# Performance work log

Measured on AMD Instinct MI355X. Metric: run time of the kernel, lower is better.

Reference implementation:

```python
import jax, jax.numpy as jnp
import numpy as np

B, N, C, H, T = 64, 4096, 768, 12, 10


def setup_inputs() -> dict:
    key = jax.random.key(0)
    kx, kq, kk, kv, kp = jax.random.split(key, 5)
    std = 0.02  # trunc_normal std from _init_weights
    return {
        "x": jax.random.normal(kx, (B, N, C), jnp.float32),
        "Wq": std * jax.random.normal(kq, (C, C), jnp.float32),
        "Wk": std * jax.random.normal(kk, (C, C), jnp.float32),
        "Wv": std * jax.random.normal(kv, (C, C), jnp.float32),
        "Wp": std * jax.random.normal(kp, (C, C), jnp.float32),
        "bp": jnp.zeros((C,), jnp.float32),
        "nb_task_tokens": T,
    }


def reference(x, Wq, Wk, Wv, Wp, bp, nb_task_tokens):
    Bq, Nq, Cq = x.shape
    d = Cq // H
    scale = d ** -0.5
    Tt = nb_task_tokens
    # q only from the first T (task) tokens; k, v from all N tokens
    q = (x[:, :Tt] @ Wq).reshape(Bq, Tt, H, d).transpose(0, 2, 1, 3) * scale  # [B,H,T,d]
    k = (x @ Wk).reshape(Bq, Nq, H, d).transpose(0, 2, 1, 3)                  # [B,H,N,d]
    v = (x @ Wv).reshape(Bq, Nq, H, d).transpose(0, 2, 1, 3)                  # [B,H,N,d]
    attn = jnp.einsum("bhtd,bhnd->bhtn", q, k)                                # [B,H,T,N]
    # mask: task token i may attend to itself and to all patch tokens (cols >= T),
    # but not to other task tokens
    rows = jnp.arange(Tt)[:, None]
    cols = jnp.arange(Nq)[None, :]
    allowed = (cols >= Tt) | (cols == rows)                                   # [T,N]
    attn = jnp.where(allowed, attn, -jnp.inf)
    attn = jax.nn.softmax(attn, axis=-1)
    x_cls = jnp.einsum("bhtn,bhnd->bhtd", attn, v)                            # [B,H,T,d]
    x_cls = x_cls.transpose(0, 2, 1, 3).reshape(Bq, Tt, Cq)
    x_cls = x_cls @ Wp + bp
    return (x_cls, attn, v)
```

## Files before the change

### kernel.cpp

```cpp
#include <hip/hip_runtime.h>

typedef __attribute__((ext_vector_type(8))) short short8;
typedef __attribute__((ext_vector_type(4))) short short4v;
typedef __attribute__((ext_vector_type(4))) float f32x4;

__device__ __forceinline__ unsigned short f2bf(float f) {
  union { float f; unsigned u; } v; v.f = f;
  unsigned r = v.u + 0x7FFFu + ((v.u >> 16) & 1u);
  return (unsigned short)(r >> 16);
}

__device__ __forceinline__ void gload16(const void* g, void* l) {
  __builtin_amdgcn_global_load_lds(
      (const __attribute__((address_space(1))) void*)g,
      (__attribute__((address_space(3))) void*)l, 16, 0, 0);
}

__global__ __launch_bounds__(256) void conv_x(const float* __restrict__ x,
                                              unsigned short* __restrict__ xb) {
  const long total = 25165824;
  long stride = (long)gridDim.x * 256;
  for (long u = blockIdx.x * 256 + threadIdx.x; u < total; u += stride) {
    const float* p = x + u * 8;
    float4 a = *(const float4*)p;
    float4 b = *(const float4*)(p + 4);
    short8 h;
    h[0] = (short)f2bf(a.x); h[1] = (short)f2bf(a.y);
    h[2] = (short)f2bf(a.z); h[3] = (short)f2bf(a.w);
    h[4] = (short)f2bf(b.x); h[5] = (short)f2bf(b.y);
    h[6] = (short)f2bf(b.z); h[7] = (short)f2bf(b.w);
    *(short8*)(xb + u * 8) = h;
  }
}

__global__ __launch_bounds__(256) void prep_w(const float* __restrict__ Wk,
                                              const float* __restrict__ Wv,
                                              unsigned short* __restrict__ Wt) {
  int idx = blockIdx.x * 256 + threadIdx.x;
  int n = idx / 768, k = idx - n * 768;
  float w = (n < 768) ? Wk[k * 768 + n] : Wv[k * 768 + (n - 768)];
  Wt[idx] = f2bf(w);
}

__global__ __launch_bounds__(256) void q_proj(const float* __restrict__ x,
                                              const float* __restrict__ Wq,
                                              unsigned short* __restrict__ q_ws) {
  int b = blockIdx.x, tid = threadIdx.x;
  __shared__ float xr[7680];
  const float* xp = x + (long)b * 4096 * 768;
  for (int i = tid; i < 7680; i += 256) xr[i] = xp[i];
  for (int i = tid; i < 12 * 6 * 64; i += 256) {
    int h = i / 384, rem = i - h * 384;
    int t = 10 + rem / 64, d = rem & 63;
    q_ws[(((long)(b * 12 + h) * 16 + t) << 6) + d] = 0;
  }
  __syncthreads();
  float acc[10][3];
#pragma unroll
  for (int t = 0; t < 10; ++t) { acc[t][0] = 0.f; acc[t][1] = 0.f; acc[t][2] = 0.f; }
  for (int k = 0; k < 768; ++k) {
    const float* wr = Wq + (long)k * 768;
    float w0 = wr[tid], w1 = wr[tid + 256], w2 = wr[tid + 512];
#pragma unroll
    for (int t = 0; t < 10; ++t) {
      float xv = xr[t * 768 + k];
      acc[t][0] += xv * w0; acc[t][1] += xv * w1; acc[t][2] += xv * w2;
    }
  }
#pragma unroll
  for (int t = 0; t < 10; ++t) {
#pragma unroll
    for (int j = 0; j < 3; ++j) {
      int c = tid + j * 256;
      int h = c >> 6, d = c & 63;
      q_ws[(((long)(b * 12 + h) * 16 + t) << 6) + d] = f2bf(acc[t][j] * 0.125f);
    }
  }
}

__global__ __launch_bounds__(512, 2) void gemm_kv7(const unsigned short* __restrict__ xb,
                                                   const unsigned short* __restrict__ Wt,
                                                   unsigned short* __restrict__ k_ws,
                                                   float* __restrict__ v_out) {
  __shared__ char smem[98304];
#define AB(i) ((unsigned short*)(smem + (i) * 16384))

  int bid = blockIdx.x;
  int lb = (bid & 7) * 768 + (bid >> 3);
  int mt = lb / 6, nt = lb - mt * 6;
  long m0 = (long)mt * 256; int n0 = nt * 256;
  int tid = threadIdx.x, lane = tid & 63;
  int uw = __builtin_amdgcn_readfirstlane(tid >> 6);
  int wm = uw >> 2, wn = uw & 3;
  int r16 = lane & 15, gk = lane >> 4;

  const unsigned short* xs = xb + m0 * 768;
  const unsigned short* wp = Wt + (long)n0 * 768;

  int srow = lane >> 2;
  int schunk = ((lane & 3) ^ ((srow >> 1) & 3)) << 3;
  const unsigned short* pA = xs + (long)(uw * 16 + srow) * 768 + schunk;
  const unsigned short* pB = wp + (long)(uw * 16 + srow) * 768 + schunk;
  const long JROW = 128 * 768;

  int rc = (gk ^ ((r16 >> 1) & 3)) << 3;

  f32x4 acc[8][4];
#pragma unroll
  for (int i = 0; i < 8; ++i)
#pragma unroll
    for (int j = 0; j < 4; ++j) acc[i][j] = (f32x4){0.f, 0.f, 0.f, 0.f};

#define STAGE(BUF, OFF)                                                         \
  {                                                                             \
    gload16(pA + (OFF), AB(2 * (BUF)) + uw * 512);                              \
    gload16(pA + (OFF) + JROW, AB(2 * (BUF)) + uw * 512 + 4096);                \
    gload16(pB + (OFF), AB(2 * (BUF) + 1) + uw * 512);                          \
    gload16(pB + (OFF) + JROW, AB(2 * (BUF) + 1) + uw * 512 + 4096);            \
  }
#define COMPUTE(BUF)                                                            \
  {                                                                             \
    const unsigned short* Ab = AB(2 * (BUF));                                   \
    const unsigned short* Bb = AB(2 * (BUF) + 1);                               \
    short8 af[8], bfr[4];                                                       \
    _Pragma("unroll")                                                           \
    for (int mi = 0; mi < 8; ++mi)                                              \
      af[mi] = *(const short8*)&Ab[(wm * 128 + mi * 16 + r16) * 32 + rc];       \
    _Pragma("unroll")                                                           \
    for (int ni = 0; ni < 4; ++ni)                                              \
      bfr[ni] = *(const short8*)&Bb[(wn * 64 + ni * 16 + r16) * 32 + rc];       \
    _Pragma("unroll")                                                           \
    for (int mi = 0; mi < 8; ++mi)                                              \
      _Pragma("unroll")                                                         \
      for (int ni = 0; ni < 4; ++ni)                                            \
        acc[mi][ni] = __builtin_amdgcn_mfma_f32_16x16x32_bf16(af[mi], bfr[ni],  \
                                                              acc[mi][ni], 0, 0, 0); \
  }
#define WB4 asm volatile("s_waitcnt vmcnt(4) lgkmcnt(0)\n\ts_barrier" ::: "memory")
#define WB0 asm volatile("s_waitcnt vmcnt(0) lgkmcnt(0)\n\ts_barrier" ::: "memory")

  STAGE(0, 0);
  STAGE(1, 32);
  WB4;

#pragma unroll 1
  for (int g = 0; g < 7; ++g) {
    STAGE(2, 64);  COMPUTE(0); WB4;
    STAGE(0, 96);  COMPUTE(1); WB4;
    STAGE(1, 128); COMPUTE(2); WB4;
    pA += 96; pB += 96;
  }
  STAGE(2, 64); COMPUTE(0); WB4;
  COMPUTE(1); WB0;
  COMPUTE(2);

#undef STAGE
#undef COMPUTE
#undef WB4
#undef WB0

  float* scr = (float*)smem + uw * 1088;
  bool is_k = (n0 < 768);
  int h = (is_k ? (n0 >> 6) : ((n0 - 768) >> 6)) + wn;
  int bq = (int)(m0 >> 12);
  int nb = (int)(m0 & 4095) + wm * 128;

#pragma unroll
  for (int mi = 0; mi < 8; ++mi) {
#pragma unroll
    for (int ni = 0; ni < 4; ++ni)
#pragma unroll
      for (int r = 0; r < 4; ++r)
        scr[(gk * 4 + r) * 68 + ni * 16 + r16] = acc[mi][ni][r];
    int nbase = nb + mi * 16;
    if (is_k) {
#pragma unroll
      for (int p = 0; p < 2; ++p) {
        int row = p * 8 + (lane >> 3), d0 = (lane & 7) << 3;
        float4 aa = *(const float4*)&scr[row * 68 + d0];
        float4 bb = *(const float4*)&scr[row * 68 + d0 + 4];
        short8 hh;
        hh[0] = (short)f2bf(aa.x); hh[1] = (short)f2bf(aa.y);
        hh[2] = (short)f2bf(aa.z); hh[3] = (short)f2bf(aa.w);
        hh[4] = (short)f2bf(bb.x); hh[5] = (short)f2bf(bb.y);
        hh[6] = (short)f2bf(bb.z); hh[7] = (short)f2bf(bb.w);
        *(short8*)&k_ws[((long)(bq * 12 + h) * 4096 + nbase + row) * 64 + d0] = hh;
      }
    } else {
#pragma unroll
      for (int p = 0; p < 4; ++p) {
        int row = p * 4 + (lane >> 4), d0 = (lane & 15) << 2;
        float4 aa = *(const float4*)&scr[row * 68 + d0];
        *(float4*)&v_out[((long)(bq * 12 + h) * 4096 + nbase + row) * 64 + d0] = aa;
      }
    }
  }
#undef AB
}

__global__ __launch_bounds__(256) void gemm_kv(const float* __restrict__ x,
                                               const unsigned short* __restrict__ Wt,
                                               unsigned short* __restrict__ k_ws,
                                               float* __restrict__ v_out) {
  __shared__ char lds[32768];
  int bid = blockIdx.x;
  int lb = (bid & 7) * 3072 + (bid >> 3);
  int mt = lb / 12, nt = lb - mt * 12;
  long m0 = (long)mt * 128; int n0 = nt * 128;
  int tid = threadIdx.x, lane = tid & 63;
  int wid = tid >> 6, wm = wid >> 1, wn = wid & 1;
  int rlo = lane & 15, gk = lane >> 4;

  const float* xs = x + m0 * 768;
  const unsigned short* wp = Wt + (long)n0 * 768;

  int arow0 = tid >> 3, ak4 = (tid & 7) << 2;
  int bn = tid >> 1, bg = (tid & 1) << 1;

  f32x4 acc[4][4];
#pragma unroll
  for (int i = 0; i < 4; ++i)
#pragma unroll
    for (int j = 0; j < 4; ++j) acc[i][j] = (f32x4){0.f, 0.f, 0.f, 0.f};

  float4 fA[4]; short8 wB[2];
#pragma unroll
  for (int it = 0; it < 4; ++it) {
    int row = it * 32 + arow0;
    fA[it] = *(const float4*)(xs + (long)row * 768 + ak4);
  }
#pragma unroll
  for (int i = 0; i < 2; ++i)
    wB[i] = *(const short8*)(wp + (long)bn * 768 + (bg + i) * 8);
#pragma unroll
  for (int it = 0; it < 4; ++it) {
    int row = it * 32 + arow0;
    short4v h;
    h[0] = (short)f2bf(fA[it].x); h[1] = (short)f2bf(fA[it].y);
    h[2] = (short)f2bf(fA[it].z); h[3] = (short)f2bf(fA[it].w);
    *(short4v*)(lds + row * 64 + ((ak4 * 2) ^ (((row >> 1) & 3) << 4))) = h;
  }
#pragma unroll
  for (int i = 0; i < 2; ++i)
    *(short8*)(lds + 16384 + bn * 64 + (((bg + i) * 16) ^ (((bn >> 1) & 3) << 4))) = wB[i];
  __syncthreads();

#pragma unroll 2
  for (int ks = 0; ks < 24; ++ks) {
    char* Ab = lds + (ks & 1) * 8192;
    char* Bb = lds + 16384 + (ks & 1) * 8192;
    bool pf = (ks + 1 < 24);
    if (pf) {
#pragma unroll
      for (int it = 0; it < 4; ++it) {
        int row = it * 32 + arow0;
        fA[it] = *(const float4*)(xs + (long)row * 768 + (ks + 1) * 32 + ak4);
      }
#pragma unroll
      for (int i = 0; i < 2; ++i)
        wB[i] = *(const short8*)(wp + (long)bn * 768 + (ks + 1) * 32 + (bg + i) * 8);
    }
    short8 af[4], bfr[4];
#pragma unroll
    for (int mi = 0; mi < 4; ++mi) {
      int row = wm * 64 + mi * 16 + rlo;
      af[mi] = *(const short8*)(Ab + row * 64 + ((gk * 16) ^ (((row >> 1) & 3) << 4)));
    }
#pragma unroll
    for (int ni = 0; ni < 4; ++ni) {
      int n = wn * 64 + ni * 16 + rlo;
      bfr[ni] = *(const short8*)(Bb + n * 64 + ((gk * 16) ^ (((n >> 1) & 3) << 4)));
    }
#pragma unroll
    for (int mi = 0; mi < 4; ++mi)
#pragma unroll
      for (int ni = 0; ni < 4; ++ni)
        acc[mi][ni] = __builtin_amdgcn_mfma_f32_16x16x32_bf16(af[mi], bfr[ni], acc[mi][ni], 0, 0, 0);
    if (pf) {
      char* An = lds + ((ks + 1) & 1) * 8192;
      char* Bn = lds + 16384 + ((ks + 1) & 1) * 8192;
#pragma unroll
      for (int it = 0; it < 4; ++it) {
        int row = it * 32 + arow0;
        short4v h;
        h[0] = (short)f2bf(fA[it].x); h[1] = (short)f2bf(fA[it].y);
        h[2] = (short)f2bf(fA[it].z); h[3] = (short)f2bf(fA[it].w);
        *(short4v*)(An + row * 64 + ((ak4 * 2) ^ (((row >> 1) & 3) << 4))) = h;
      }
#pragma unroll
      for (int i = 0; i < 2; ++i)
        *(short8*)(Bn + bn * 64 + (((bg + i) * 16) ^ (((bn >> 1) & 3) << 4))) = wB[i];
    }
    __syncthreads();
  }

  bool is_k = (n0 < 768);
  int cb = is_k ? n0 : n0 - 768;
#pragma unroll
  for (int ni = 0; ni < 4; ++ni) {
    int cc = cb + wn * 64 + ni * 16 + rlo;
    int h = cc >> 6, d = cc & 63;
#pragma unroll
    for (int mi = 0; mi < 4; ++mi) {
#pragma unroll
      for (int r = 0; r < 4; ++r) {
        long m = m0 + wm * 64 + mi * 16 + gk * 4 + r;
        int b = (int)(m >> 12), n = (int)(m & 4095);
        long off = ((long)(b * 12 + h) * 4096 + n) * 64 + d;
        float val = acc[mi][ni][r];
        if (is_k) k_ws[off] = f2bf(val);
        else      v_out[off] = val;
      }
    }
  }
}

__global__ __launch_bounds__(512) void attn_fused(const unsigned short* __restrict__ k_ws,
                                                  const unsigned short* __restrict__ q_ws,
                                                  const float* __restrict__ v_glob,
                                                  float* __restrict__ attn_out,
                                                  float* __restrict__ preproj) {
  __shared__ float red[8][16];
  __shared__ float rowmax[16];
  __shared__ float rowinv[16];
  __shared__ float scratch[8 * 256];

  int tid = threadIdx.x, lane = tid & 63, w = tid >> 6;
  int bh = blockIdx.x;
  int r16 = lane & 15, gk = lane >> 4;
  int trc = (r16 < 10) ? r16 : 9;

  const unsigned short* kp = k_ws + (long)bh * (4096 * 64);
  const unsigned short* qp = q_ws + (long)bh * 1024;
  float* sraw = attn_out + (long)bh * 40960;
  const float* vp = v_glob + (long)bh * (4096 * 64);

  short8 qf0 = *(const short8*)(qp + r16 * 64 + gk * 8);
  short8 qf1 = *(const short8*)(qp + r16 * 64 + 32 + gk * 8);

  float pmax = -3.0e38f;
  for (int ch = 0; ch < 32; ++ch) {
    int n0 = (w * 32 + ch) << 4;
    short8 kf0 = *(const short8*)(kp + (long)(n0 + r16) * 64 + gk * 8);
    short8 kf1 = *(const short8*)(kp + (long)(n0 + r16) * 64 + 32 + gk * 8);
    f32x4 d4 = (f32x4){0.f, 0.f, 0.f, 0.f};
    d4 = __builtin_amdgcn_mfma_f32_16x16x32_bf16(kf0, qf0, d4, 0, 0, 0);
    d4 = __builtin_amdgcn_mfma_f32_16x16x32_bf16(kf1, qf1, d4, 0, 0, 0);
    float sv[4];
#pragma unroll
    for (int r = 0; r < 4; ++r) {
      int n = n0 + gk * 4 + r;
      float s = d4[r];
      if (n < 10 && n != r16) s = -1e30f;
      sv[r] = s;
      pmax = fmaxf(pmax, s);
    }
    if (r16 < 10)
      *(float4*)(sraw + r16 * 4096 + n0 + gk * 4) = make_float4(sv[0], sv[1], sv[2], sv[3]);
  }
  pmax = fmaxf(pmax, __shfl_xor(pmax, 16));
  pmax = fmaxf(pmax, __shfl_xor(pmax, 32));
  if (lane < 16) red[w][lane] = pmax;
  __syncthreads();
  if (tid < 16) {
    float m = red[0][tid];
#pragma unroll
    for (int i = 1; i < 8; ++i) m = fmaxf(m, red[i][tid]);
    rowmax[tid] = m;
  }
  __syncthreads();

  float mx = rowmax[trc];
  float psum = 0.f;
  for (int ch = 0; ch < 16; ++ch) {
    int n0 = ((w * 16 + ch) << 5) + gk * 8;
    float4 a = *(const float4*)(sraw + trc * 4096 + n0);
    float4 b2 = *(const float4*)(sraw + trc * 4096 + n0 + 4);
    psum += __expf(a.x - mx) + __expf(a.y - mx) + __expf(a.z - mx) + __expf(a.w - mx)
          + __expf(b2.x - mx) + __expf(b2.y - mx) + __expf(b2.z - mx) + __expf(b2.w - mx);
  }
  psum += __shfl_xor(psum, 16);
  psum += __shfl_xor(psum, 32);
  if (lane < 16) red[w][lane] = psum;
  __syncthreads();
  if (tid < 16) {
    float s = 0.f;
#pragma unroll
    for (int i = 0; i < 8; ++i) s += red[i][tid];
    rowinv[tid] = 1.0f / s;
  }
  __syncthreads();

  int dc = w & 3, half = w >> 2;
  int d0 = dc << 4;
  float inv = rowinv[trc];
  f32x4 acc = (f32x4){0.f, 0.f, 0.f, 0.f};
  for (int kk = 0; kk < 64; ++kk) {
    int nr = half * 2048 + kk * 32 + gk * 8;
    float* sp = sraw + trc * 4096 + nr;
    float4 s0 = *(const float4*)(sp);
    float4 s1 = *(const float4*)(sp + 4);
    float p0 = __expf(s0.x - mx) * inv, p1 = __expf(s0.y - mx) * inv;
    float p2 = __expf(s0.z - mx) * inv, p3 = __expf(s0.w - mx) * inv;
    float p4 = __expf(s1.x - mx) * inv, p5 = __expf(s1.y - mx) * inv;
    float p6 = __expf(s1.z - mx) * inv, p7 = __expf(s1.w - mx) * inv;
    if (r16 < 10) {
      *(float4*)(sp)     = make_float4(p0, p1, p2, p3);
      *(float4*)(sp + 4) = make_float4(p4, p5, p6, p7);
    }
    short8 pa;
    pa[0] = (short)f2bf(p0); pa[1] = (short)f2bf(p1);
    pa[2] = (short)f2bf(p2); pa[3] = (short)f2bf(p3);
    pa[4] = (short)f2bf(p4); pa[5] = (short)f2bf(p5);
    pa[6] = (short)f2bf(p6); pa[7] = (short)f2bf(p7);
    short8 vb;
    const float* vrow = vp + (long)nr * 64 + d0 + r16;
#pragma unroll
    for (int j = 0; j < 8; ++j) vb[j] = (short)f2bf(vrow[j * 64]);
    acc = __builtin_amdgcn_mfma_f32_16x16x32_bf16(pa, vb, acc, 0, 0, 0);
  }
#pragma unroll
  for (int r = 0; r < 4; ++r)
    scratch[w * 256 + (gk * 4 + r) * 16 + r16] = acc[r];
  __syncthreads();

  int b = bh / 12, h = bh - b * 12;
  for (int idx = tid; idx < 640; idx += 512) {
    int tt = idx >> 6, d = idx & 63;
    int c = d >> 4, dl = d & 15;
    float s = scratch[c * 256 + tt * 16 + dl] + scratch[(c + 4) * 256 + tt * 16 + dl];
    preproj[((long)b * 10 + tt) * 768 + h * 64 + d] = s;
  }
}

__global__ __launch_bounds__(256) void proj_out_k(const float* __restrict__ preproj,
                                                  const float* __restrict__ Wp,
                                                  const float* __restrict__ bp,
                                                  float* __restrict__ out0) {
  int b = blockIdx.x, tid = threadIdx.x;
  __shared__ float xr[7680];
  const float* pp = preproj + (long)b * 7680;
  for (int i = tid; i < 7680; i += 256) xr[i] = pp[i];
  __syncthreads();
  float acc[10][3];
#pragma unroll
  for (int t = 0; t < 10; ++t) { acc[t][0] = 0.f; acc[t][1] = 0.f; acc[t][2] = 0.f; }
  for (int k = 0; k < 768; ++k) {
    const float* wr = Wp + (long)k * 768;
    float w0 = wr[tid], w1 = wr[tid + 256], w2 = wr[tid + 512];
#pragma unroll
    for (int t = 0; t < 10; ++t) {
      float xv = xr[t * 768 + k];
      acc[t][0] += xv * w0; acc[t][1] += xv * w1; acc[t][2] += xv * w2;
    }
  }
  float b0 = bp[tid], b1 = bp[tid + 256], b2 = bp[tid + 512];
  float* op = out0 + (long)b * 7680;
#pragma unroll
  for (int t = 0; t < 10; ++t) {
    op[t * 768 + tid]       = acc[t][0] + b0;
    op[t * 768 + tid + 256] = acc[t][1] + b1;
    op[t * 768 + tid + 512] = acc[t][2] + b2;
  }
}

extern "C" void kernel_launch(void* const* d_in, const int* in_sizes, int n_in,
                              void* d_out, int out_size, void* d_ws, size_t ws_size,
                              hipStream_t stream) {
  (void)in_sizes; (void)n_in; (void)out_size;
  const float* x  = (const float*)d_in[0];
  const float* Wq = (const float*)d_in[1];
  const float* Wk = (const float*)d_in[2];
  const float* Wv = (const float*)d_in[3];
  const float* Wp = (const float*)d_in[4];
  const float* bp = (const float*)d_in[5];

  float* out      = (float*)d_out;
  float* attn_out = out + 491520;
  float* v_out    = out + 31948800;

  char* ws = (char*)d_ws;
  const size_t NEED_BIG = 811204608;

  if (ws_size >= NEED_BIG) {
    unsigned short* x_bf16 = (unsigned short*)(ws);
    unsigned short* k_ws = (unsigned short*)(ws + 402653184);
    unsigned short* q_ws = (unsigned short*)(ws + 805306368);
    unsigned short* Wt   = (unsigned short*)(ws + 806879232);
    float* preproj       = (float*)(ws + 809238528);

    conv_x<<<dim3(2048), dim3(256), 0, stream>>>(x, x_bf16);
    prep_w<<<dim3(4608), dim3(256), 0, stream>>>(Wk, Wv, Wt);
    q_proj<<<dim3(64), dim3(256), 0, stream>>>(x, Wq, q_ws);
    gemm_kv7<<<dim3(6144), dim3(512), 0, stream>>>(x_bf16, Wt, k_ws, v_out);
    attn_fused<<<dim3(768), dim3(512), 0, stream>>>(k_ws, q_ws, v_out, attn_out, preproj);
    proj_out_k<<<dim3(64), dim3(256), 0, stream>>>(preproj, Wp, bp, out);
  } else {
    unsigned short* k_ws = (unsigned short*)(ws);
    unsigned short* q_ws = (unsigned short*)(ws + 402653184);
    unsigned short* Wt   = (unsigned short*)(ws + 404226048);
    float* preproj       = (float*)(ws + 406585344);

    prep_w<<<dim3(4608), dim3(256), 0, stream>>>(Wk, Wv, Wt);
    q_proj<<<dim3(64), dim3(256), 0, stream>>>(x, Wq, q_ws);
    gemm_kv<<<dim3(24576), dim3(256), 0, stream>>>(x, Wt, k_ws, v_out);
    attn_fused<<<dim3(768), dim3(512), 0, stream>>>(k_ws, q_ws, v_out, attn_out, preproj);
    proj_out_k<<<dim3(64), dim3(256), 0, stream>>>(preproj, Wp, bp, out);
  }
}
```

Baseline: 1.617 ms.

## Restructure KV GEMM main loop into 8-wave ping-pong with BK=64 double buffering

The KV projection GEMM now uses 64-wide K tiles with two LDS buffers instead of three 32-wide buffers. It also uses a new 8-chunk XOR swizzle. Each K step is split into four sub-phases that interleave LDS fragment reads and global-to-LDS prefetches with MFMA bursts, separated by barriers and s_setprio. The aim is to hide memory latency and keep the matrix units busy. LDS per block grows to 128KB, which likely limits the kernel to one block per CU and so reduces occupancy.

```diff
diff --git a/kernel.cpp b/kernel.cpp
--- a/kernel.cpp
+++ b/kernel.cpp
@@ -78,12 +78,15 @@
   }
 }
 
-__global__ __launch_bounds__(512, 2) void gemm_kv7(const unsigned short* __restrict__ xb,
+__global__ __launch_bounds__(512, 2) void gemm_kv8(const unsigned short* __restrict__ xb,
                                                    const unsigned short* __restrict__ Wt,
                                                    unsigned short* __restrict__ k_ws,
                                                    float* __restrict__ v_out) {
-  __shared__ char smem[98304];
-#define AB(i) ((unsigned short*)(smem + (i) * 16384))
+  __shared__ char smem[131072];
+#define A0T ((unsigned short*)(smem))
+#define B0T ((unsigned short*)(smem + 32768))
+#define A1T ((unsigned short*)(smem + 65536))
+#define B1T ((unsigned short*)(smem + 98304))
 
   int bid = blockIdx.x;
   int lb = (bid & 7) * 768 + (bid >> 3);
@@ -97,13 +100,15 @@
   const unsigned short* xs = xb + m0 * 768;
   const unsigned short* wp = Wt + (long)n0 * 768;
 
-  int srow = lane >> 2;
-  int schunk = ((lane & 3) ^ ((srow >> 1) & 3)) << 3;
-  const unsigned short* pA = xs + (long)(uw * 16 + srow) * 768 + schunk;
-  const unsigned short* pB = wp + (long)(uw * 16 + srow) * 768 + schunk;
-  const long JROW = 128 * 768;
-
-  int rc = (gk ^ ((r16 >> 1) & 3)) << 3;
+  int srow8 = lane >> 3;
+  int sch = ((lane & 7) ^ (srow8 & 7)) << 3;
+  const unsigned short* sA = xs + (long)(uw * 8 + srow8) * 768 + sch;
+  const unsigned short* sB = wp + (long)(uw * 8 + srow8) * 768 + sch;
+
+  int ck0 = ((gk ^ (r16 & 7)) << 3);
+  int ck1 = (((4 + gk) ^ (r16 & 7)) << 3);
+  int arb = (wm * 128 + r16) * 64;
+  int brb = (wn * 64 + r16) * 64;
 
   f32x4 acc[8][4];
 #pragma unroll
@@ -111,53 +116,100 @@
 #pragma unroll
     for (int j = 0; j < 4; ++j) acc[i][j] = (f32x4){0.f, 0.f, 0.f, 0.f};
 
-#define STAGE(BUF, OFF)                                                         \
+#define SGA(AT, I, KO) gload16(sA + (long)(I) * 49152 + (KO), (AT) + ((I) * 64 + uw * 8) * 64)
+#define SGB(BT, I, KO) gload16(sB + (long)(I) * 49152 + (KO), (BT) + ((I) * 64 + uw * 8) * 64)
+#define WBND asm volatile("s_waitcnt vmcnt(0)\n\ts_barrier" ::: "memory")
+#define PBAR __builtin_amdgcn_s_barrier()
+
+#define BODY(AC, BC, AN, BN, KOS, DOST)                                         \
   {                                                                             \
-    gload16(pA + (OFF), AB(2 * (BUF)) + uw * 512);                              \
-    gload16(pA + (OFF) + JROW, AB(2 * (BUF)) + uw * 512 + 4096);                \
-    gload16(pB + (OFF), AB(2 * (BUF) + 1) + uw * 512);                          \
-    gload16(pB + (OFF) + JROW, AB(2 * (BUF) + 1) + uw * 512 + 4096);            \
-  }
-#define COMPUTE(BUF)                                                            \
-  {                                                                             \
-    const unsigned short* Ab = AB(2 * (BUF));                                   \
-    const unsigned short* Bb = AB(2 * (BUF) + 1);                               \
-    short8 af[8], bfr[4];                                                       \
-    _Pragma("unroll")                                                           \
-    for (int mi = 0; mi < 8; ++mi)                                              \
-      af[mi] = *(const short8*)&Ab[(wm * 128 + mi * 16 + r16) * 32 + rc];       \
-    _Pragma("unroll")                                                           \
-    for (int ni = 0; ni < 4; ++ni)                                              \
-      bfr[ni] = *(const short8*)&Bb[(wn * 64 + ni * 16 + r16) * 32 + rc];       \
-    _Pragma("unroll")                                                           \
-    for (int mi = 0; mi < 8; ++mi)                                              \
+    short8 fa[4][2], fb0[2][2], fb1[2][2];                                      \
+                    \
+    if (DOST) { SGA(AN, 0, KOS); SGA(AN, 1, KOS); SGB(BN, 0, KOS); SGB(BN, 1, KOS); } \
+    _Pragma("unroll")                                                           \
+    for (int mi = 0; mi < 4; ++mi) {                                            \
+      fa[mi][0] = *(const short8*)&AC[arb + mi * 1024 + ck0];                   \
+      fa[mi][1] = *(const short8*)&AC[arb + mi * 1024 + ck1];                   \
+    }                                                                           \
+    _Pragma("unroll")                                                           \
+    for (int ni = 0; ni < 2; ++ni) {                                            \
+      fb0[ni][0] = *(const short8*)&BC[brb + ni * 1024 + ck0];                  \
+      fb0[ni][1] = *(const short8*)&BC[brb + ni * 1024 + ck1];                  \
+    }                                                                           \
+    PBAR;                                                                       \
+    __builtin_amdgcn_s_setprio(1);                                              \
+    _Pragma("unroll")                                                           \
+    for (int mi = 0; mi < 4; ++mi)                                              \
       _Pragma("unroll")                                                         \
-      for (int ni = 0; ni < 4; ++ni)                                            \
-        acc[mi][ni] = __builtin_amdgcn_mfma_f32_16x16x32_bf16(af[mi], bfr[ni],  \
-                                                              acc[mi][ni], 0, 0, 0); \
-  }
-#define WB4 asm volatile("s_waitcnt vmcnt(4) lgkmcnt(0)\n\ts_barrier" ::: "memory")
-#define WB0 asm volatile("s_waitcnt vmcnt(0) lgkmcnt(0)\n\ts_barrier" ::: "memory")
-
-  STAGE(0, 0);
-  STAGE(1, 32);
-  WB4;
+      for (int ni = 0; ni < 2; ++ni) {                                          \
+        acc[mi][ni] = __builtin_amdgcn_mfma_f32_16x16x32_bf16(fa[mi][0], fb0[ni][0], acc[mi][ni], 0, 0, 0); \
+        acc[mi][ni] = __builtin_amdgcn_mfma_f32_16x16x32_bf16(fa[mi][1], fb0[ni][1], acc[mi][ni], 0, 0, 0); \
+      }                                                                         \
+    __builtin_amdgcn_s_setprio(0);                                              \
+    PBAR;                                                                       \
+                           \
+    if (DOST) { SGA(AN, 2, KOS); SGA(AN, 3, KOS); SGB(BN, 2, KOS); SGB(BN, 3, KOS); } \
+    _Pragma("unroll")                                                           \
+    for (int ni = 0; ni < 2; ++ni) {                                            \
+      fb1[ni][0] = *(const short8*)&BC[brb + (ni + 2) * 1024 + ck0];            \
+      fb1[ni][1] = *(const short8*)&BC[brb + (ni + 2) * 1024 + ck1];            \
+    }                                                                           \
+    PBAR;                                                                       \
+    __builtin_amdgcn_s_setprio(1);                                              \
+    _Pragma("unroll")                                                           \
+    for (int mi = 0; mi < 4; ++mi)                                              \
+      _Pragma("unroll")                                                         \
+      for (int ni = 0; ni < 2; ++ni) {                                          \
+        acc[mi][ni + 2] = __builtin_amdgcn_mfma_f32_16x16x32_bf16(fa[mi][0], fb1[ni][0], acc[mi][ni + 2], 0, 0, 0); \
+        acc[mi][ni + 2] = __builtin_amdgcn_mfma_f32_16x16x32_bf16(fa[mi][1], fb1[ni][1], acc[mi][ni + 2], 0, 0, 0); \
+      }                                                                         \
+    __builtin_amdgcn_s_setprio(0);                                              \
+    PBAR;                                                                       \
+                                       \
+    _Pragma("unroll")                                                           \
+    for (int mi = 0; mi < 4; ++mi) {                                            \
+      fa[mi][0] = *(const short8*)&AC[arb + (mi + 4) * 1024 + ck0];             \
+      fa[mi][1] = *(const short8*)&AC[arb + (mi + 4) * 1024 + ck1];             \
+    }                                                                           \
+    PBAR;                                                                       \
+    __builtin_amdgcn_s_setprio(1);                                              \
+    _Pragma("unroll")                                                           \
+    for (int mi = 0; mi < 4; ++mi)                                              \
+      _Pragma("unroll")                                                         \
+      for (int ni = 0; ni < 2; ++ni) {                                          \
+        acc[mi + 4][ni + 2] = __builtin_amdgcn_mfma_f32_16x16x32_bf16(fa[mi][0], fb1[ni][0], acc[mi + 4][ni + 2], 0, 0, 0); \
+        acc[mi + 4][ni + 2] = __builtin_amdgcn_mfma_f32_16x16x32_bf16(fa[mi][1], fb1[ni][1], acc[mi + 4][ni + 2], 0, 0, 0); \
+      }                                                                         \
+    __builtin_amdgcn_s_setprio(0);                                              \
+    PBAR;                                                                       \
+                                 \
+    __builtin_amdgcn_s_setprio(1);                                              \
+    _Pragma("unroll")                                                           \
+    for (int mi = 0; mi < 4; ++mi)                                              \
+      _Pragma("unroll")                                                         \
+      for (int ni = 0; ni < 2; ++ni) {                                          \
+        acc[mi + 4][ni] = __builtin_amdgcn_mfma_f32_16x16x32_bf16(fa[mi][0], fb0[ni][0], acc[mi + 4][ni], 0, 0, 0); \
+        acc[mi + 4][ni] = __builtin_amdgcn_mfma_f32_16x16x32_bf16(fa[mi][1], fb0[ni][1], acc[mi + 4][ni], 0, 0, 0); \
+      }                                                                         \
+    __builtin_amdgcn_s_setprio(0);                                              \
+  }
+
+  SGA(A0T, 0, 0); SGA(A0T, 1, 0); SGA(A0T, 2, 0); SGA(A0T, 3, 0);
+  SGB(B0T, 0, 0); SGB(B0T, 1, 0); SGB(B0T, 2, 0); SGB(B0T, 3, 0);
+  WBND;
 
 #pragma unroll 1
-  for (int g = 0; g < 7; ++g) {
-    STAGE(2, 64);  COMPUTE(0); WB4;
-    STAGE(0, 96);  COMPUTE(1); WB4;
-    STAGE(1, 128); COMPUTE(2); WB4;
-    pA += 96; pB += 96;
-  }
-  STAGE(2, 64); COMPUTE(0); WB4;
-  COMPUTE(1); WB0;
-  COMPUTE(2);
-
-#undef STAGE
-#undef COMPUTE
-#undef WB4
-#undef WB0
+  for (int t = 0; t < 12; t += 2) {
+    BODY(A0T, B0T, A1T, B1T, (t + 1) * 64, true);
+    WBND;
+    BODY(A1T, B1T, A0T, B0T, (t + 2) * 64, (t + 2) < 12);
+    WBND;
+  }
+#undef BODY
+#undef SGA
+#undef SGB
+#undef WBND
+#undef PBAR
 
   float* scr = (float*)smem + uw * 1088;
   bool is_k = (n0 < 768);
@@ -195,7 +247,10 @@
       }
     }
   }
-#undef AB
+#undef A0T
+#undef B0T
+#undef A1T
+#undef B1T
 }
 
 __global__ __launch_bounds__(256) void gemm_kv(const float* __restrict__ x,
@@ -492,7 +547,7 @@
     conv_x<<<dim3(2048), dim3(256), 0, stream>>>(x, x_bf16);
     prep_w<<<dim3(4608), dim3(256), 0, stream>>>(Wk, Wv, Wt);
     q_proj<<<dim3(64), dim3(256), 0, stream>>>(x, Wq, q_ws);
-    gemm_kv7<<<dim3(6144), dim3(512), 0, stream>>>(x_bf16, Wt, k_ws, v_out);
+    gemm_kv8<<<dim3(6144), dim3(512), 0, stream>>>(x_bf16, Wt, k_ws, v_out);
     attn_fused<<<dim3(768), dim3(512), 0, stream>>>(k_ws, q_ws, v_out, attn_out, preproj);
     proj_out_k<<<dim3(64), dim3(256), 0, stream>>>(preproj, Wp, bp, out);
   } else {
```

Measured after the change: 1.606 ms. Within noise of the previous version (-0.7%).
